# Optimization experiments

Hardware: AMD Instinct MI355X
Metric: run time of the kernel (lower is better)

## Reference

```python
import jax, jax.numpy as jnp
import numpy as np

B, S, D, H = 2, 2048, 1024, 16
HD = D // H


def setup_inputs() -> dict:
    key = jax.random.key(0)
    ks = jax.random.split(key, 9)
    s = 1.0 / np.sqrt(D)
    return {
        "x": jax.random.normal(ks[0], (B, S, D), dtype=jnp.float32),
        "Wq": jax.random.uniform(ks[1], (D, D), jnp.float32, -s, s),
        "bq": jax.random.uniform(ks[2], (D,), jnp.float32, -s, s),
        "Wk": jax.random.uniform(ks[3], (D, D), jnp.float32, -s, s),
        "bk": jax.random.uniform(ks[4], (D,), jnp.float32, -s, s),
        "Wv": jax.random.uniform(ks[5], (D, D), jnp.float32, -s, s),
        "bv": jax.random.uniform(ks[6], (D,), jnp.float32, -s, s),
        "Wo": jax.random.uniform(ks[7], (D, D), jnp.float32, -s, s),
        "bo": jax.random.uniform(ks[8], (D,), jnp.float32, -s, s),
    }


def reference(x, Wq, bq, Wk, bk, Wv, bv, Wo, bo):
    # QKV projections: [B,S,D] -> [B,H,S,HD]
    def split_heads(t):
        return t.reshape(B, S, H, HD).transpose(0, 2, 1, 3)

    Q = split_heads(x @ Wq + bq)
    K = split_heads(x @ Wk + bk)
    V = split_heads(x @ Wv + bv)

    scale = 1.0 / np.sqrt(HD).astype(np.float32)
    scores = jnp.einsum("bhqd,bhkd->bhqk", Q, K) * scale  # [B,H,S,S]
    attn = jax.nn.softmax(scores, axis=-1)
    out = jnp.einsum("bhqk,bhkd->bhqd", attn, V)  # [B,H,S,HD]
    out = out.transpose(0, 2, 1, 3).reshape(B, S, D)
    return out @ Wo + bo
```

## Files before the change

kernel.cpp:

```cpp
#include <hip/hip_runtime.h>
#include <hip/hip_bf16.h>

#define B_ 2
#define S_ 2048
#define D_ 1024
#define H_ 16
#define HD_ 64
#define M_ (B_ * S_)

#define SC2L 0.18033688011112042f

typedef __attribute__((ext_vector_type(8))) short short8;
typedef __attribute__((ext_vector_type(4))) float f32x4;
using bf16_t = __hip_bfloat16;

__device__ __forceinline__ float fast_exp2(float x) { return __builtin_amdgcn_exp2f(x); }

__device__ __forceinline__ short f2bfs(float f) {
    __hip_bfloat16 h = __float2bfloat16(f);
    return *reinterpret_cast<short*>(&h);
}

typedef __attribute__((address_space(1))) const unsigned int gl_u32;
typedef __attribute__((address_space(3))) unsigned int lds_u32;

__device__ __forceinline__ void gl_lds16(const bf16_t* g, bf16_t* l) {
    __builtin_amdgcn_global_load_lds((gl_u32*)g, (lds_u32*)l, 16, 0, 0);
}

__device__ __forceinline__ int swzb(int row, int colbyte) {
    return (row << 7) + (colbyte ^ ((row & 7) << 4));
}

__device__ __forceinline__ int swz32(int row, int chunk) {
    return (row << 6) + ((chunk ^ ((row >> 1) & 3)) << 4);
}

__global__ __launch_bounds__(256) void k_prep(const float* __restrict__ x,
                                              const float* __restrict__ W0,
                                              const float* __restrict__ W1,
                                              const float* __restrict__ W2,
                                              const float* __restrict__ W3,
                                              bf16_t* __restrict__ xb,
                                              bf16_t* T0, bf16_t* T1, bf16_t* T2, bf16_t* T3) {
    const int z = blockIdx.z;
    const int tx = threadIdx.x, ty = threadIdx.y;
    if (z == 4) {
        const int blk = blockIdx.y * 32 + blockIdx.x;
        const int tid = ty * 32 + tx;
        int i = blk * 4096 + tid * 16;
#pragma unroll
        for (int half = 0; half < 2; ++half) {
            float4 f0 = ((const float4*)(x + i))[0];
            float4 f1 = ((const float4*)(x + i))[1];
            short8 v;
            v[0] = f2bfs(f0.x); v[1] = f2bfs(f0.y); v[2] = f2bfs(f0.z); v[3] = f2bfs(f0.w);
            v[4] = f2bfs(f1.x); v[5] = f2bfs(f1.y); v[6] = f2bfs(f1.z); v[7] = f2bfs(f1.w);
            *(short8*)(xb + i) = v;
            i += 8;
        }
        return;
    }
    __shared__ float tile[32][33];
    const float* W = z == 0 ? W0 : z == 1 ? W1 : z == 2 ? W2 : W3;
    bf16_t* Wt = z == 0 ? T0 : z == 1 ? T1 : z == 2 ? T2 : T3;
    const int n0 = blockIdx.x * 32, k0 = blockIdx.y * 32;
#pragma unroll
    for (int r = 0; r < 4; ++r)
        tile[ty + 8 * r][tx] = W[(size_t)(k0 + ty + 8 * r) * D_ + n0 + tx];
    __syncthreads();
#pragma unroll
    for (int r = 0; r < 4; ++r)
        Wt[(size_t)(n0 + ty + 8 * r) * D_ + k0 + tx] = __float2bfloat16(tile[tx][ty + 8 * r]);
}

__device__ __forceinline__ void stage_pair32(const bf16_t* __restrict__ Asrc,
                                             const bf16_t* __restrict__ Bsrc,
                                             int k0, int tid,
                                             bf16_t* Ab, bf16_t* Bb) {
#pragma unroll
    for (int c = 0; c < 2; ++c) {
        int idx = c * 256 + tid;
        int r = idx >> 2, ch = idx & 3;
        int cs = ch ^ ((r >> 1) & 3);
        gl_lds16(Asrc + (size_t)r * D_ + k0 + cs * 8, Ab + idx * 8);
        gl_lds16(Bsrc + (size_t)r * D_ + k0 + cs * 8, Bb + idx * 8);
    }
}

__device__ __forceinline__ void gemm_compute32(const bf16_t* Ab, const bf16_t* Bb,
                                               int lane, int wr, int wc, f32x4 acc[4][4]) {
    const char* AbC = (const char*)Ab;
    const char* BbC = (const char*)Bb;
    const int g = lane >> 4;
    short8 af[4], bf[4];
    const int arow = wr * 64 + (lane & 15);
    const int brow = wc * 64 + (lane & 15);
#pragma unroll
    for (int i = 0; i < 4; ++i) af[i] = *(const short8*)(AbC + swz32(arow + i * 16, g));
#pragma unroll
    for (int j = 0; j < 4; ++j) bf[j] = *(const short8*)(BbC + swz32(brow + j * 16, g));
#pragma unroll
    for (int i = 0; i < 4; ++i)
#pragma unroll
        for (int j = 0; j < 4; ++j)
            acc[i][j] = __builtin_amdgcn_mfma_f32_16x16x32_bf16(af[i], bf[j], acc[i][j], 0, 0, 0);
}

#define GEMM_KLOOP(ASRC, BSRC)                                                   \
    stage_pair32(ASRC, BSRC, 0, tid, Ab[0], Bb[0]);                              \
    stage_pair32(ASRC, BSRC, 32, tid, Ab[1], Bb[1]);                             \
    constexpr int NS = D_ / 32;                                                  \
    _Pragma("unroll 3")                                                          \
    for (int step = 0; step < NS - 1; ++step) {                                  \
        asm volatile("s_waitcnt vmcnt(4)" ::: "memory");                         \
        __builtin_amdgcn_s_barrier();                                            \
        if (step + 2 < NS)                                                       \
            stage_pair32(ASRC, BSRC, (step + 2) * 32, tid,                       \
                         Ab[(step + 2) % 3], Bb[(step + 2) % 3]);                \
        gemm_compute32(Ab[step % 3], Bb[step % 3], lane, wr, wc, acc);           \
    }                                                                            \
    asm volatile("s_waitcnt vmcnt(0)" ::: "memory");                             \
    __builtin_amdgcn_s_barrier();                                                \
    gemm_compute32(Ab[(NS - 1) % 3], Bb[(NS - 1) % 3], lane, wr, wc, acc);

__global__ __launch_bounds__(256, 4) void k_qkv(const bf16_t* __restrict__ xb,
                                                const bf16_t* __restrict__ Wtq,
                                                const bf16_t* __restrict__ Wtk,
                                                const bf16_t* __restrict__ Wtv,
                                                const float* __restrict__ bq,
                                                const float* __restrict__ bk,
                                                const float* __restrict__ bv,
                                                bf16_t* __restrict__ Qh,
                                                bf16_t* __restrict__ Kh,
                                                bf16_t* __restrict__ Vt) {
    __shared__ __align__(16) bf16_t Ab[3][128 * 32];
    __shared__ __align__(16) bf16_t Bb[3][128 * 32];
    const int p = blockIdx.x;
    const int v0 = (p & 7) * 96 + (p >> 3);
    const int sc = v0 % 24;
    const int sel = sc >> 3;
    const bf16_t* Bt = sel == 0 ? Wtq : sel == 1 ? Wtk : Wtv;
    const float* bias = sel == 0 ? bq : sel == 1 ? bk : bv;
    const int col0 = (sc & 7) * 128;
    const int row0 = (v0 / 24) * 128;
    const int tid = threadIdx.x, lane = tid & 63, w = tid >> 6;
    const int wr = w >> 1, wc = w & 1;
    const bf16_t* Asrc = xb + (size_t)row0 * D_;
    const bf16_t* Bsrc = Bt + (size_t)col0 * D_;

    f32x4 acc[4][4];
#pragma unroll
    for (int i = 0; i < 4; ++i)
#pragma unroll
        for (int j = 0; j < 4; ++j) acc[i][j] = (f32x4){0.f, 0.f, 0.f, 0.f};

    GEMM_KLOOP(Asrc, Bsrc)

#pragma unroll
    for (int i = 0; i < 4; ++i)
#pragma unroll
        for (int j = 0; j < 4; ++j)
#pragma unroll
            for (int r = 0; r < 4; ++r) {
                int grow = row0 + wr * 64 + i * 16 + 4 * (lane >> 4) + r;
                int gcol = col0 + wc * 64 + j * 16 + (lane & 15);
                float v = acc[i][j][r] + bias[gcol];
                int b = grow >> 11, s = grow & (S_ - 1);
                int h = gcol >> 6, hd = gcol & (HD_ - 1);
                if (sel == 0)
                    Qh[(((size_t)b * H_ + h) * S_ + s) * HD_ + hd] = __float2bfloat16(v * SC2L);
                else if (sel == 1)
                    Kh[(((size_t)b * H_ + h) * S_ + s) * HD_ + hd] = __float2bfloat16(v);
                else
                    Vt[(((size_t)b * H_ + h) * HD_ + hd) * S_ + s] = __float2bfloat16(v);
            }
}

__global__ __launch_bounds__(256, 4) void k_gemm_out(const bf16_t* __restrict__ AO,
                                                     const bf16_t* __restrict__ Wto,
                                                     const float* __restrict__ bo,
                                                     float* __restrict__ out) {
    __shared__ __align__(16) bf16_t Ab[3][128 * 32];
    __shared__ __align__(16) bf16_t Bb[3][128 * 32];
    const int p = blockIdx.x;
    const int v0 = (p & 7) * 32 + (p >> 3);
    const int col0 = (v0 & 7) * 128;
    const int row0 = (v0 >> 3) * 128;
    const int tid = threadIdx.x, lane = tid & 63, w = tid >> 6;
    const int wr = w >> 1, wc = w & 1;
    const bf16_t* Asrc = AO + (size_t)row0 * D_;
    const bf16_t* Bsrc = Wto + (size_t)col0 * D_;

    f32x4 acc[4][4];
#pragma unroll
    for (int i = 0; i < 4; ++i)
#pragma unroll
        for (int j = 0; j < 4; ++j) acc[i][j] = (f32x4){0.f, 0.f, 0.f, 0.f};

    GEMM_KLOOP(Asrc, Bsrc)

#pragma unroll
    for (int i = 0; i < 4; ++i)
#pragma unroll
        for (int j = 0; j < 4; ++j)
#pragma unroll
            for (int r = 0; r < 4; ++r) {
                int grow = row0 + wr * 64 + i * 16 + 4 * (lane >> 4) + r;
                int gcol = col0 + wc * 64 + j * 16 + (lane & 15);
                out[(size_t)grow * D_ + gcol] = acc[i][j][r] + bo[gcol];
            }
}

__global__ __launch_bounds__(512, 4) void k_attn(const bf16_t* __restrict__ Qh,
                                                 const bf16_t* __restrict__ Kh,
                                                 const bf16_t* __restrict__ Vt,
                                                 bf16_t* __restrict__ AO) {
    constexpr int NT = S_ / 64;
    __shared__ __align__(16) bf16_t Kb[3][64 * 64];
    __shared__ __align__(16) bf16_t Vb[3][64 * 64];
    __shared__ __align__(16) bf16_t Pt[8][16 * 64];
    const int tid = threadIdx.x, lane = tid & 63, w = tid >> 6;
    const int g = lane >> 4, q = lane & 15;
    const int bid = blockIdx.x;
    const int swz = (bid & 7) * 64 + (bid >> 3);
    const int qt = swz & 15, bh = swz >> 4;
    const int h = bh & 15, b = bh >> 4;
    const bf16_t* Qbase = Qh + ((size_t)bh * S_ + qt * 128 + w * 16) * HD_;
    const bf16_t* Kbase = Kh + (size_t)bh * S_ * HD_;
    const bf16_t* Vbase = Vt + (size_t)bh * HD_ * S_;
    char* PtC = (char*)Pt[w];

    auto stage = [&](int buf, int kt) {
        int r = tid >> 3, s = tid & 7;
        int lsw = s ^ (r & 7);
        gl_lds16(Kbase + (size_t)(kt * 64 + r) * HD_ + lsw * 8, &Kb[buf][tid * 8]);
        gl_lds16(Vbase + (size_t)r * S_ + kt * 64 + lsw * 8, &Vb[buf][tid * 8]);
    };

    short8 qf[2];
#pragma unroll
    for (int kc = 0; kc < 2; ++kc)
        qf[kc] = *(const short8*)(Qbase + (size_t)q * HD_ + kc * 32 + 8 * g);

    f32x4 ls4 = (f32x4){0.f, 0.f, 0.f, 0.f};
    f32x4 o[4];
#pragma unroll
    for (int c = 0; c < 4; ++c) o[c] = (f32x4){0.f, 0.f, 0.f, 0.f};

    f32x4 scA[4], scB[4];

    auto qk_tile = [&](int kt, f32x4 (&sc)[4]) {
        const char* KbC = (const char*)Kb[kt % 3];
        __builtin_amdgcn_s_setprio(1);
#pragma unroll
        for (int ktb = 0; ktb < 4; ++ktb) {
            f32x4 a = (f32x4){0.f, 0.f, 0.f, 0.f};
#pragma unroll
            for (int kc = 0; kc < 2; ++kc) {
                short8 kf = *(const short8*)(KbC + swzb(ktb * 16 + q, kc * 64 + 16 * g));
                a = __builtin_amdgcn_mfma_f32_16x16x32_bf16(kf, qf[kc], a, 0, 0, 0);
            }
            sc[ktb] = a;
        }
        __builtin_amdgcn_s_setprio(0);
    };

    auto finish_pv = [&](f32x4 (&sc)[4], int vt) {
#pragma unroll
        for (int t = 0; t < 4; ++t)
#pragma unroll
            for (int r = 0; r < 4; ++r)
                sc[t][r] = fast_exp2(sc[t][r]);
        ls4 += (sc[0] + sc[1]) + (sc[2] + sc[3]);
#pragma unroll
        for (int t = 0; t < 4; ++t) {
            short4 pk;
            pk.x = f2bfs(sc[t][0]); pk.y = f2bfs(sc[t][1]);
            pk.z = f2bfs(sc[t][2]); pk.w = f2bfs(sc[t][3]);
            *(short4*)(PtC + swzb(q, t * 32 + 8 * g)) = pk;
        }
        const char* VbC = (const char*)Vb[vt % 3];
        __builtin_amdgcn_s_setprio(1);
#pragma unroll
        for (int kc = 0; kc < 2; ++kc) {
            short8 pf = *(const short8*)(PtC + swzb(q, kc * 64 + 16 * g));
#pragma unroll
            for (int c = 0; c < 4; ++c) {
                short8 vf = *(const short8*)(VbC + swzb(c * 16 + q, kc * 64 + 16 * g));
                o[c] = __builtin_amdgcn_mfma_f32_16x16x32_bf16(vf, pf, o[c], 0, 0, 0);
            }
        }
        __builtin_amdgcn_s_setprio(0);
    };

    stage(0, 0);
    __syncthreads();
    stage(1, 1);
    qk_tile(0, scA);

#pragma unroll 1
    for (int kt = 1; kt + 1 < NT; kt += 2) {
        __syncthreads();
        stage((kt + 1) % 3, kt + 1);
        qk_tile(kt, scB);
        finish_pv(scA, kt - 1);
        __syncthreads();
        if (kt + 2 < NT) stage((kt + 2) % 3, kt + 2);
        qk_tile(kt + 1, scA);
        finish_pv(scB, kt);
    }
    __syncthreads();
    qk_tile(NT - 1, scB);
    finish_pv(scA, NT - 2);
    finish_pv(scB, NT - 1);

    float lsum = (ls4[0] + ls4[1]) + (ls4[2] + ls4[3]);
    lsum += __shfl_xor(lsum, 16);
    lsum += __shfl_xor(lsum, 32);
    float rls = __builtin_amdgcn_rcpf(lsum);
#pragma unroll
    for (int c = 0; c < 4; ++c) {
        short4 ok;
        ok.x = f2bfs(o[c][0] * rls); ok.y = f2bfs(o[c][1] * rls);
        ok.z = f2bfs(o[c][2] * rls); ok.w = f2bfs(o[c][3] * rls);
        *(short4*)(PtC + swzb(q, c * 32 + 8 * g)) = ok;
    }
    const int tok = qt * 128 + w * 16 + (lane >> 2);
    const int dch = (lane & 3) * 32;
    short8 r0 = *(const short8*)(PtC + swzb(lane >> 2, dch));
    short8 r1 = *(const short8*)(PtC + swzb(lane >> 2, dch + 16));
    bf16_t* dst = AO + ((size_t)b * S_ + tok) * D_ + h * HD_ + (lane & 3) * 16;
    *(short8*)dst = r0;
    *(short8*)(dst + 8) = r1;
}

extern "C" void kernel_launch(void* const* d_in, const int* in_sizes, int n_in,
                              void* d_out, int out_size, void* d_ws, size_t ws_size,
                              hipStream_t stream) {
    const float* x  = (const float*)d_in[0];
    const float* Wq = (const float*)d_in[1];
    const float* bq = (const float*)d_in[2];
    const float* Wk = (const float*)d_in[3];
    const float* bk = (const float*)d_in[4];
    const float* Wv = (const float*)d_in[5];
    const float* bv = (const float*)d_in[6];
    const float* Wo = (const float*)d_in[7];
    const float* bo = (const float*)d_in[8];

    char* ws = (char*)d_ws;
    const size_t MB = 1024 * 1024;
    bf16_t* Wtq = (bf16_t*)(ws + 0 * MB);
    bf16_t* Wtk = (bf16_t*)(ws + 2 * MB);
    bf16_t* Wtv = (bf16_t*)(ws + 4 * MB);
    bf16_t* Wto = (bf16_t*)(ws + 6 * MB);
    bf16_t* xb  = (bf16_t*)(ws + 8 * MB);
    bf16_t* Qh  = (bf16_t*)(ws + 16 * MB);
    bf16_t* Kh  = (bf16_t*)(ws + 24 * MB);
    bf16_t* Vt  = (bf16_t*)(ws + 32 * MB);
    bf16_t* AO  = (bf16_t*)(ws + 8 * MB);

    k_prep<<<dim3(32, 32, 5), dim3(32, 8), 0, stream>>>(x, Wq, Wk, Wv, Wo, xb, Wtq, Wtk, Wtv, Wto);
    k_qkv<<<768, 256, 0, stream>>>(xb, Wtq, Wtk, Wtv, bq, bk, bv, Qh, Kh, Vt);
    k_attn<<<B_ * H_ * (S_ / 128), 512, 0, stream>>>(Qh, Kh, Vt, AO);
    k_gemm_out<<<256, 256, 0, stream>>>(AO, Wto, bo, (float*)d_out);
}
```

Before: 113.8 us.

## Switch attention to 32x32 MFMA with 4 waves of 32 queries each

```diff
diff --git a/kernel.cpp b/kernel.cpp
--- a/kernel.cpp
+++ b/kernel.cpp
@@ -12,6 +12,7 @@
 
 typedef __attribute__((ext_vector_type(8))) short short8;
 typedef __attribute__((ext_vector_type(4))) float f32x4;
+typedef __attribute__((ext_vector_type(16))) float f32x16;
 using bf16_t = __hip_bfloat16;
 
 __device__ __forceinline__ float fast_exp2(float x) { return __builtin_amdgcn_exp2f(x); }
@@ -212,127 +213,125 @@
             }
 }
 
-__global__ __launch_bounds__(512, 4) void k_attn(const bf16_t* __restrict__ Qh,
+__global__ __launch_bounds__(256, 2) void k_attn(const bf16_t* __restrict__ Qh,
                                                  const bf16_t* __restrict__ Kh,
                                                  const bf16_t* __restrict__ Vt,
                                                  bf16_t* __restrict__ AO) {
     constexpr int NT = S_ / 64;
-    __shared__ __align__(16) bf16_t Kb[3][64 * 64];
-    __shared__ __align__(16) bf16_t Vb[3][64 * 64];
-    __shared__ __align__(16) bf16_t Pt[8][16 * 64];
+    __shared__ __align__(16) bf16_t Kb[2][64 * 64];
+    __shared__ __align__(16) bf16_t Vb[2][64 * 64];
+    __shared__ __align__(16) bf16_t Pt[4][32 * 64];
     const int tid = threadIdx.x, lane = tid & 63, w = tid >> 6;
-    const int g = lane >> 4, q = lane & 15;
+    const int q32 = lane & 31, hh = lane >> 5;
     const int bid = blockIdx.x;
     const int swz = (bid & 7) * 64 + (bid >> 3);
     const int qt = swz & 15, bh = swz >> 4;
     const int h = bh & 15, b = bh >> 4;
-    const bf16_t* Qbase = Qh + ((size_t)bh * S_ + qt * 128 + w * 16) * HD_;
+    const bf16_t* Qbase = Qh + ((size_t)bh * S_ + qt * 128 + w * 32) * HD_;
     const bf16_t* Kbase = Kh + (size_t)bh * S_ * HD_;
     const bf16_t* Vbase = Vt + (size_t)bh * HD_ * S_;
     char* PtC = (char*)Pt[w];
 
+    auto psl = [&](int row, int slot, int sub) -> char* {
+        return PtC + row * 128 + ((slot ^ (row & 7)) << 4) + sub;
+    };
+
     auto stage = [&](int buf, int kt) {
-        int r = tid >> 3, s = tid & 7;
-        int lsw = s ^ (r & 7);
-        gl_lds16(Kbase + (size_t)(kt * 64 + r) * HD_ + lsw * 8, &Kb[buf][tid * 8]);
-        gl_lds16(Vbase + (size_t)r * S_ + kt * 64 + lsw * 8, &Vb[buf][tid * 8]);
+#pragma unroll
+        for (int c = 0; c < 2; ++c) {
+            int idx = c * 256 + tid;
+            int r = idx >> 3, s = idx & 7;
+            int lsw = s ^ (r & 7);
+            gl_lds16(Kbase + (size_t)(kt * 64 + r) * HD_ + lsw * 8, &Kb[buf][idx * 8]);
+            gl_lds16(Vbase + (size_t)r * S_ + kt * 64 + lsw * 8, &Vb[buf][idx * 8]);
+        }
     };
 
-    short8 qf[2];
-#pragma unroll
-    for (int kc = 0; kc < 2; ++kc)
-        qf[kc] = *(const short8*)(Qbase + (size_t)q * HD_ + kc * 32 + 8 * g);
+    short8 qf[4];
+#pragma unroll
+    for (int ds = 0; ds < 4; ++ds)
+        qf[ds] = *(const short8*)(Qbase + (size_t)q32 * HD_ + ds * 16 + 8 * hh);
 
     f32x4 ls4 = (f32x4){0.f, 0.f, 0.f, 0.f};
-    f32x4 o[4];
-#pragma unroll
-    for (int c = 0; c < 4; ++c) o[c] = (f32x4){0.f, 0.f, 0.f, 0.f};
-
-    f32x4 scA[4], scB[4];
-
-    auto qk_tile = [&](int kt, f32x4 (&sc)[4]) {
-        const char* KbC = (const char*)Kb[kt % 3];
-        __builtin_amdgcn_s_setprio(1);
-#pragma unroll
-        for (int ktb = 0; ktb < 4; ++ktb) {
-            f32x4 a = (f32x4){0.f, 0.f, 0.f, 0.f};
-#pragma unroll
-            for (int kc = 0; kc < 2; ++kc) {
-                short8 kf = *(const short8*)(KbC + swzb(ktb * 16 + q, kc * 64 + 16 * g));
-                a = __builtin_amdgcn_mfma_f32_16x16x32_bf16(kf, qf[kc], a, 0, 0, 0);
-            }
-            sc[ktb] = a;
-        }
-        __builtin_amdgcn_s_setprio(0);
-    };
-
-    auto finish_pv = [&](f32x4 (&sc)[4], int vt) {
-#pragma unroll
-        for (int t = 0; t < 4; ++t)
-#pragma unroll
-            for (int r = 0; r < 4; ++r)
-                sc[t][r] = fast_exp2(sc[t][r]);
-        ls4 += (sc[0] + sc[1]) + (sc[2] + sc[3]);
-#pragma unroll
-        for (int t = 0; t < 4; ++t) {
-            short4 pk;
-            pk.x = f2bfs(sc[t][0]); pk.y = f2bfs(sc[t][1]);
-            pk.z = f2bfs(sc[t][2]); pk.w = f2bfs(sc[t][3]);
-            *(short4*)(PtC + swzb(q, t * 32 + 8 * g)) = pk;
-        }
-        const char* VbC = (const char*)Vb[vt % 3];
-        __builtin_amdgcn_s_setprio(1);
-#pragma unroll
-        for (int kc = 0; kc < 2; ++kc) {
-            short8 pf = *(const short8*)(PtC + swzb(q, kc * 64 + 16 * g));
-#pragma unroll
-            for (int c = 0; c < 4; ++c) {
-                short8 vf = *(const short8*)(VbC + swzb(c * 16 + q, kc * 64 + 16 * g));
-                o[c] = __builtin_amdgcn_mfma_f32_16x16x32_bf16(vf, pf, o[c], 0, 0, 0);
-            }
-        }
-        __builtin_amdgcn_s_setprio(0);
-    };
+    f32x16 o0 = {}, o1 = {};
 
     stage(0, 0);
     __syncthreads();
-    stage(1, 1);
-    qk_tile(0, scA);
-
-#pragma unroll 1
-    for (int kt = 1; kt + 1 < NT; kt += 2) {
+
+#pragma unroll 2
+    for (int kt = 0; kt < NT; ++kt) {
+        const int cur = kt & 1;
+        if (kt + 1 < NT) stage(cur ^ 1, kt + 1);
+        const char* KbC = (const char*)Kb[cur];
+        const char* VbC = (const char*)Vb[cur];
+
+        f32x16 s0 = {}, s1 = {};
+        __builtin_amdgcn_s_setprio(1);
+#pragma unroll
+        for (int ds = 0; ds < 4; ++ds) {
+            const int cb = ds * 32 + 16 * hh;
+            short8 k0 = *(const short8*)(KbC + swzb(q32, cb));
+            short8 k1 = *(const short8*)(KbC + swzb(32 + q32, cb));
+            s0 = __builtin_amdgcn_mfma_f32_32x32x16_bf16(k0, qf[ds], s0, 0, 0, 0);
+            s1 = __builtin_amdgcn_mfma_f32_32x32x16_bf16(k1, qf[ds], s1, 0, 0, 0);
+        }
+        __builtin_amdgcn_s_setprio(0);
+
+#pragma unroll
+        for (int r = 0; r < 16; ++r) {
+            s0[r] = fast_exp2(s0[r]);
+            s1[r] = fast_exp2(s1[r]);
+        }
+#pragma unroll
+        for (int r = 0; r < 16; ++r) ls4[r & 3] += s0[r] + s1[r];
+
+#pragma unroll
+        for (int j = 0; j < 4; ++j) {
+            short4 p0, p1;
+            p0.x = f2bfs(s0[4 * j + 0]); p0.y = f2bfs(s0[4 * j + 1]);
+            p0.z = f2bfs(s0[4 * j + 2]); p0.w = f2bfs(s0[4 * j + 3]);
+            p1.x = f2bfs(s1[4 * j + 0]); p1.y = f2bfs(s1[4 * j + 1]);
+            p1.z = f2bfs(s1[4 * j + 2]); p1.w = f2bfs(s1[4 * j + 3]);
+            *(short4*)psl(q32, j, 8 * hh) = p0;
+            *(short4*)psl(q32, j + 4, 8 * hh) = p1;
+        }
+
+        __builtin_amdgcn_s_setprio(1);
+#pragma unroll
+        for (int ks = 0; ks < 4; ++ks) {
+            short8 pv = *(const short8*)psl(q32, 2 * ks + hh, 0);
+            const int cb = ks * 32 + 16 * hh;
+            short8 v0 = *(const short8*)(VbC + swzb(q32, cb));
+            short8 v1 = *(const short8*)(VbC + swzb(32 + q32, cb));
+            o0 = __builtin_amdgcn_mfma_f32_32x32x16_bf16(v0, pv, o0, 0, 0, 0);
+            o1 = __builtin_amdgcn_mfma_f32_32x32x16_bf16(v1, pv, o1, 0, 0, 0);
+        }
+        __builtin_amdgcn_s_setprio(0);
         __syncthreads();
-        stage((kt + 1) % 3, kt + 1);
-        qk_tile(kt, scB);
-        finish_pv(scA, kt - 1);
-        __syncthreads();
-        if (kt + 2 < NT) stage((kt + 2) % 3, kt + 2);
-        qk_tile(kt + 1, scA);
-        finish_pv(scB, kt);
-    }
-    __syncthreads();
-    qk_tile(NT - 1, scB);
-    finish_pv(scA, NT - 2);
-    finish_pv(scB, NT - 1);
+    }
 
     float lsum = (ls4[0] + ls4[1]) + (ls4[2] + ls4[3]);
-    lsum += __shfl_xor(lsum, 16);
     lsum += __shfl_xor(lsum, 32);
     float rls = __builtin_amdgcn_rcpf(lsum);
 #pragma unroll
-    for (int c = 0; c < 4; ++c) {
-        short4 ok;
-        ok.x = f2bfs(o[c][0] * rls); ok.y = f2bfs(o[c][1] * rls);
-        ok.z = f2bfs(o[c][2] * rls); ok.w = f2bfs(o[c][3] * rls);
-        *(short4*)(PtC + swzb(q, c * 32 + 8 * g)) = ok;
-    }
-    const int tok = qt * 128 + w * 16 + (lane >> 2);
-    const int dch = (lane & 3) * 32;
-    short8 r0 = *(const short8*)(PtC + swzb(lane >> 2, dch));
-    short8 r1 = *(const short8*)(PtC + swzb(lane >> 2, dch + 16));
-    bf16_t* dst = AO + ((size_t)b * S_ + tok) * D_ + h * HD_ + (lane & 3) * 16;
-    *(short8*)dst = r0;
-    *(short8*)(dst + 8) = r1;
+    for (int j = 0; j < 4; ++j) {
+        short4 w0, w1;
+        w0.x = f2bfs(o0[4 * j + 0] * rls); w0.y = f2bfs(o0[4 * j + 1] * rls);
+        w0.z = f2bfs(o0[4 * j + 2] * rls); w0.w = f2bfs(o0[4 * j + 3] * rls);
+        w1.x = f2bfs(o1[4 * j + 0] * rls); w1.y = f2bfs(o1[4 * j + 1] * rls);
+        w1.z = f2bfs(o1[4 * j + 2] * rls); w1.w = f2bfs(o1[4 * j + 3] * rls);
+        *(short4*)psl(q32, j, 8 * hh) = w0;
+        *(short4*)psl(q32, j + 4, 8 * hh) = w1;
+    }
+    const int r = lane >> 1;
+    const int half = lane & 1;
+    const int tok = qt * 128 + w * 32 + r;
+    bf16_t* dst = AO + ((size_t)b * S_ + tok) * D_ + h * HD_ + half * 32;
+#pragma unroll
+    for (int c2 = 0; c2 < 4; ++c2) {
+        short8 rr = *(const short8*)psl(r, half * 4 + c2, 0);
+        *(short8*)(dst + c2 * 8) = rr;
+    }
 }
 
 extern "C" void kernel_launch(void* const* d_in, const int* in_sizes, int n_in,
@@ -362,6 +361,6 @@
 
     k_prep<<<dim3(32, 32, 5), dim3(32, 8), 0, stream>>>(x, Wq, Wk, Wv, Wo, xb, Wtq, Wtk, Wtv, Wto);
     k_qkv<<<768, 256, 0, stream>>>(xb, Wtq, Wtk, Wtv, bq, bk, bv, Qh, Kh, Vt);
-    k_attn<<<B_ * H_ * (S_ / 128), 512, 0, stream>>>(Qh, Kh, Vt, AO);
+    k_attn<<<B_ * H_ * (S_ / 128), 256, 0, stream>>>(Qh, Kh, Vt, AO);
     k_gemm_out<<<256, 256, 0, stream>>>(AO, Wto, bo, (float*)d_out);
 }
```

New measurement: 117.0 us. 1.03x slower.

## Enlarge QKV GEMM tile to 128x256 with per-wave 128x64 subtiles

Applied to the files above, without the earlier changes.

```diff
diff --git a/kernel.cpp b/kernel.cpp
--- a/kernel.cpp
+++ b/kernel.cpp
@@ -107,24 +107,7 @@
             acc[i][j] = __builtin_amdgcn_mfma_f32_16x16x32_bf16(af[i], bf[j], acc[i][j], 0, 0, 0);
 }
 
-#define GEMM_KLOOP(ASRC, BSRC)                                                   \
-    stage_pair32(ASRC, BSRC, 0, tid, Ab[0], Bb[0]);                              \
-    stage_pair32(ASRC, BSRC, 32, tid, Ab[1], Bb[1]);                             \
-    constexpr int NS = D_ / 32;                                                  \
-    _Pragma("unroll 3")                                                          \
-    for (int step = 0; step < NS - 1; ++step) {                                  \
-        asm volatile("s_waitcnt vmcnt(4)" ::: "memory");                         \
-        __builtin_amdgcn_s_barrier();                                            \
-        if (step + 2 < NS)                                                       \
-            stage_pair32(ASRC, BSRC, (step + 2) * 32, tid,                       \
-                         Ab[(step + 2) % 3], Bb[(step + 2) % 3]);                \
-        gemm_compute32(Ab[step % 3], Bb[step % 3], lane, wr, wc, acc);           \
-    }                                                                            \
-    asm volatile("s_waitcnt vmcnt(0)" ::: "memory");                             \
-    __builtin_amdgcn_s_barrier();                                                \
-    gemm_compute32(Ab[(NS - 1) % 3], Bb[(NS - 1) % 3], lane, wr, wc, acc);
-
-__global__ __launch_bounds__(256, 4) void k_qkv(const bf16_t* __restrict__ xb,
+__global__ __launch_bounds__(256, 2) void k_qkv(const bf16_t* __restrict__ xb,
                                                 const bf16_t* __restrict__ Wtq,
                                                 const bf16_t* __restrict__ Wtk,
                                                 const bf16_t* __restrict__ Wtv,
@@ -135,36 +118,94 @@
                                                 bf16_t* __restrict__ Kh,
                                                 bf16_t* __restrict__ Vt) {
     __shared__ __align__(16) bf16_t Ab[3][128 * 32];
-    __shared__ __align__(16) bf16_t Bb[3][128 * 32];
+    __shared__ __align__(16) bf16_t Bb[3][256 * 32];
     const int p = blockIdx.x;
-    const int v0 = (p & 7) * 96 + (p >> 3);
-    const int sc = v0 % 24;
-    const int sel = sc >> 3;
+    const int v0 = (p & 7) * 48 + (p >> 3);
+    const int rowgrp = v0 / 12;
+    const int ct = v0 % 12;
+    const int sel = ct >> 2;
     const bf16_t* Bt = sel == 0 ? Wtq : sel == 1 ? Wtk : Wtv;
     const float* bias = sel == 0 ? bq : sel == 1 ? bk : bv;
-    const int col0 = (sc & 7) * 128;
-    const int row0 = (v0 / 24) * 128;
+    const int col0 = (ct & 3) * 256;
+    const int row0 = rowgrp * 128;
     const int tid = threadIdx.x, lane = tid & 63, w = tid >> 6;
-    const int wr = w >> 1, wc = w & 1;
     const bf16_t* Asrc = xb + (size_t)row0 * D_;
     const bf16_t* Bsrc = Bt + (size_t)col0 * D_;
 
-    f32x4 acc[4][4];
-#pragma unroll
-    for (int i = 0; i < 4; ++i)
+    auto stage = [&](int buf, int k0) {
+#pragma unroll
+        for (int c = 0; c < 2; ++c) {
+            int idx = c * 256 + tid;
+            int r = idx >> 2, ch = idx & 3;
+            int cs = ch ^ ((r >> 1) & 3);
+            gl_lds16(Asrc + (size_t)r * D_ + k0 + cs * 8, Ab[buf] + idx * 8);
+        }
+#pragma unroll
+        for (int c = 0; c < 4; ++c) {
+            int idx = c * 256 + tid;
+            int r = idx >> 2, ch = idx & 3;
+            int cs = ch ^ ((r >> 1) & 3);
+            gl_lds16(Bsrc + (size_t)r * D_ + k0 + cs * 8, Bb[buf] + idx * 8);
+        }
+    };
+
+    f32x4 acc[8][4];
+#pragma unroll
+    for (int i = 0; i < 8; ++i)
 #pragma unroll
         for (int j = 0; j < 4; ++j) acc[i][j] = (f32x4){0.f, 0.f, 0.f, 0.f};
 
-    GEMM_KLOOP(Asrc, Bsrc)
-
-#pragma unroll
-    for (int i = 0; i < 4; ++i)
+    stage(0, 0);
+    stage(1, 32);
+    constexpr int NS = D_ / 32;
+    const int g = lane >> 4;
+#pragma unroll 3
+    for (int step = 0; step < NS - 1; ++step) {
+        asm volatile("s_waitcnt vmcnt(6)" ::: "memory");
+        __builtin_amdgcn_s_barrier();
+        if (step + 2 < NS) stage((step + 2) % 3, (step + 2) * 32);
+        const char* AbC = (const char*)Ab[step % 3];
+        const char* BbC = (const char*)Bb[step % 3];
+        short8 af[8], bf[4];
+#pragma unroll
+        for (int i = 0; i < 8; ++i)
+            af[i] = *(const short8*)(AbC + swz32(i * 16 + (lane & 15), g));
 #pragma unroll
         for (int j = 0; j < 4; ++j)
+            bf[j] = *(const short8*)(BbC + swz32(w * 64 + j * 16 + (lane & 15), g));
+#pragma unroll
+        for (int i = 0; i < 8; ++i)
+#pragma unroll
+            for (int j = 0; j < 4; ++j)
+                acc[i][j] = __builtin_amdgcn_mfma_f32_16x16x32_bf16(af[i], bf[j], acc[i][j], 0, 0, 0);
+    }
+    asm volatile("s_waitcnt vmcnt(0)" ::: "memory");
+    __builtin_amdgcn_s_barrier();
+    {
+        const char* AbC = (const char*)Ab[(NS - 1) % 3];
+        const char* BbC = (const char*)Bb[(NS - 1) % 3];
+        short8 af[8], bf[4];
+#pragma unroll
+        for (int i = 0; i < 8; ++i)
+            af[i] = *(const short8*)(AbC + swz32(i * 16 + (lane & 15), g));
+#pragma unroll
+        for (int j = 0; j < 4; ++j)
+            bf[j] = *(const short8*)(BbC + swz32(w * 64 + j * 16 + (lane & 15), g));
+#pragma unroll
+        for (int i = 0; i < 8; ++i)
+#pragma unroll
+            for (int j = 0; j < 4; ++j)
+                acc[i][j] = __builtin_amdgcn_mfma_f32_16x16x32_bf16(af[i], bf[j], acc[i][j], 0, 0, 0);
+    }
+
+#pragma unroll
+    for (int i = 0; i < 8; ++i)
+#pragma unroll
+        for (int j = 0; j < 4; ++j)
 #pragma unroll
             for (int r = 0; r < 4; ++r) {
-                int grow = row0 + wr * 64 + i * 16 + 4 * (lane >> 4) + r;
-                int gcol = col0 + wc * 64 + j * 16 + (lane & 15);
+                int grow = row0 + i * 16 + 4 * (lane >> 4) + r;
+                int gcol = col0 + w * 64 + j * 16 + (lane & 15);
                 float v = acc[i][j][r] + bias[gcol];
                 int b = grow >> 11, s = grow & (S_ - 1);
                 int h = gcol >> 6, hd = gcol & (HD_ - 1);
@@ -198,7 +239,21 @@
 #pragma unroll
         for (int j = 0; j < 4; ++j) acc[i][j] = (f32x4){0.f, 0.f, 0.f, 0.f};
 
-    GEMM_KLOOP(Asrc, Bsrc)
+    stage_pair32(Asrc, Bsrc, 0, tid, Ab[0], Bb[0]);
+    stage_pair32(Asrc, Bsrc, 32, tid, Ab[1], Bb[1]);
+    constexpr int NS = D_ / 32;
+#pragma unroll 3
+    for (int step = 0; step < NS - 1; ++step) {
+        asm volatile("s_waitcnt vmcnt(4)" ::: "memory");
+        __builtin_amdgcn_s_barrier();
+        if (step + 2 < NS)
+            stage_pair32(Asrc, Bsrc, (step + 2) * 32, tid,
+                         Ab[(step + 2) % 3], Bb[(step + 2) % 3]);
+        gemm_compute32(Ab[step % 3], Bb[step % 3], lane, wr, wc, acc);
+    }
+    asm volatile("s_waitcnt vmcnt(0)" ::: "memory");
+    __builtin_amdgcn_s_barrier();
+    gemm_compute32(Ab[(NS - 1) % 3], Bb[(NS - 1) % 3], lane, wr, wc, acc);
 
 #pragma unroll
     for (int i = 0; i < 4; ++i)
@@ -361,7 +416,7 @@
     bf16_t* AO  = (bf16_t*)(ws + 8 * MB);
 
     k_prep<<<dim3(32, 32, 5), dim3(32, 8), 0, stream>>>(x, Wq, Wk, Wv, Wo, xb, Wtq, Wtk, Wtv, Wto);
-    k_qkv<<<768, 256, 0, stream>>>(xb, Wtq, Wtk, Wtv, bq, bk, bv, Qh, Kh, Vt);
+    k_qkv<<<384, 256, 0, stream>>>(xb, Wtq, Wtk, Wtv, bq, bk, bv, Qh, Kh, Vt);
     k_attn<<<B_ * H_ * (S_ / 128), 512, 0, stream>>>(Qh, Kh, Vt, AO);
     k_gemm_out<<<256, 256, 0, stream>>>(AO, Wto, bo, (float*)d_out);
 }
```

Result: slower. 120.7 us (+6.0%).
